# Optimization experiments

Measured on AMD Instinct MI355X. Metric: run time of the kernel, lower is better.

## Reference

```python
import jax, jax.numpy as jnp
import numpy as np

IN_DIM = 128
OUT_DIM = 128
DEGREE = 3
BATCH = 8192


def setup_inputs() -> dict:
    key = jax.random.key(0)
    k1, k2 = jax.random.split(key)
    x = jax.random.normal(k1, (BATCH, IN_DIM), dtype=jnp.float32)
    # coeff ~ 0.1*randn, shape [out_dim*in_dim, degree+1]
    coeff = 0.1 * jax.random.normal(k2, (OUT_DIM * IN_DIM, DEGREE + 1), dtype=jnp.float32)
    return {"x": x, "coeff": coeff}


def reference(x, coeff):
    # x: [B, in_dim], coeff: [out_dim*in_dim, D+1]
    # Original tiles x to [out_dim*in_dim, B]; edge i = (o*in_dim + j) uses x[:, j].
    # out[i,b] = sum_d coeff[i,d] * x[b, i % in_dim]**d, then sum over in_dim.
    B, in_dim = x.shape
    D1 = coeff.shape[-1]
    out_dim = coeff.shape[0] // in_dim
    exps = jnp.arange(D1, dtype=x.dtype)
    powed = x[:, :, None] ** exps            # [B, in_dim, D+1]
    c = coeff.reshape(out_dim, in_dim, D1)    # [out_dim, in_dim, D+1]
    # per-edge polynomial eval fused with sum over in_dim
    y = jnp.einsum('bid,oid->bo', powed, c)   # [B, out_dim]
    return y
```

## Files before the change

kernel.cpp:

```cpp
#include <hip/hip_runtime.h>


#define BATCH   8192
#define IN_DIM  128
#define OUT_DIM 128
#define KDIM    512

typedef __attribute__((ext_vector_type(8))) short bf16x8;
typedef __attribute__((ext_vector_type(4))) float f32x4;

__device__ inline unsigned short f2bf(float f) {
    union { float f; unsigned int u; } v; v.f = f;
    unsigned int u = v.u;
    u += 0x7FFFu + ((u >> 16) & 1u);
    return (unsigned short)(u >> 16);
}

#if defined(__has_builtin)
#if __has_builtin(__builtin_amdgcn_cvt_pk_bf16_f32)
#define HAVE_HW_PKBF16 1
#endif
#endif

#ifdef HAVE_HW_PKBF16
typedef __attribute__((ext_vector_type(2))) __bf16 bf16x2_t;
__device__ inline unsigned int pk2(float a, float b) {
    bf16x2_t r = __builtin_amdgcn_cvt_pk_bf16_f32(a, b);
    union { bf16x2_t v; unsigned int u; } c; c.v = r; return c.u;
}
#else
__device__ inline unsigned int pk2(float a, float b) {
    return (unsigned int)f2bf(a) | ((unsigned int)f2bf(b) << 16);
}
#endif

__global__ __launch_bounds__(256) void kan_prep(const float* __restrict__ coeff,
                                                unsigned int* __restrict__ wbf) {
    const int i = (blockIdx.x * 256 + threadIdx.x) * 4;
    const float4 c = *(const float4*)(coeff + i);
    uint2 o;
    o.x = pk2(c.x, c.y);
    o.y = pk2(c.z, c.w);
    *(uint2*)(wbf + i / 2) = o;
}

__global__ __launch_bounds__(64) void kan_mfma(const float* __restrict__ x,
                                               const unsigned short* __restrict__ wbf,
                                               float* __restrict__ out) {
    const int lane = threadIdx.x;
    const int q    = lane >> 4;
    const int r    = lane & 15;
    const int m0   = blockIdx.x * 16;
    const int n0   = blockIdx.y * 16;

    const float*          xrow = x   + (size_t)(m0 + r) * IN_DIM;
    const unsigned short* wrow = wbf + (size_t)(n0 + r) * KDIM;

    f32x4 acc = {0.f, 0.f, 0.f, 0.f};

    #pragma unroll
    for (int s = 0; s < KDIM / 32; ++s) {
        const bf16x8 bw = *(const bf16x8*)(wrow + s * 32 + q * 8);

        const float2 xv = *(const float2*)(xrow + s * 8 + q * 2);
        const float x0 = xv.x, x1 = xv.y;
        union { unsigned int u[4]; bf16x8 v; } af;
        af.u[0] = pk2(1.0f, x0);
        af.u[1] = pk2(x0 * x0, x0 * x0 * x0);
        af.u[2] = pk2(1.0f, x1);
        af.u[3] = pk2(x1 * x1, x1 * x1 * x1);

        acc = __builtin_amdgcn_mfma_f32_16x16x32_bf16(af.v, bw, acc, 0, 0, 0);
    }

    float* orow = out + (size_t)(m0 + q * 4) * OUT_DIM + n0 + r;
    #pragma unroll
    for (int rr = 0; rr < 4; ++rr) {
        orow[rr * OUT_DIM] = acc[rr];
    }
}

extern "C" void kernel_launch(void* const* d_in, const int* in_sizes, int n_in,
                              void* d_out, int out_size, void* d_ws, size_t ws_size,
                              hipStream_t stream) {
    const float* x     = (const float*)d_in[0];
    const float* coeff = (const float*)d_in[1];
    float* out = (float*)d_out;

    unsigned int* wbf = (unsigned int*)d_ws;

    kan_prep<<<OUT_DIM * KDIM / (256 * 4), 256, 0, stream>>>(coeff, wbf);

    dim3 grid(BATCH / 16, OUT_DIM / 16);
    kan_mfma<<<grid, 64, 0, stream>>>(x, (const unsigned short*)wbf, out);
}
```

Before: 72.21 us.

## Fuse coefficient bf16 conversion into MFMA kernel and tile two N blocks

Drops the separate prep kernel that converted coeff to bf16 in workspace. The main kernel now loads fp32 coefficients directly and converts them in registers. Each wave also computes two 16-wide output tiles, so the x-power fragment is reused across two MFMAs and the grid is halved in N. This removes a kernel launch and a workspace round trip, but doubles coefficient bytes read per block and repeats the conversion in every block.

```diff
diff --git a/kernel.cpp b/kernel.cpp
--- a/kernel.cpp
+++ b/kernel.cpp
@@ -34,49 +34,61 @@
 }
 #endif
 
-__global__ __launch_bounds__(256) void kan_prep(const float* __restrict__ coeff,
-                                                unsigned int* __restrict__ wbf) {
-    const int i = (blockIdx.x * 256 + threadIdx.x) * 4;
-    const float4 c = *(const float4*)(coeff + i);
-    uint2 o;
-    o.x = pk2(c.x, c.y);
-    o.y = pk2(c.z, c.w);
-    *(uint2*)(wbf + i / 2) = o;
+union frag_u { unsigned int u[4]; bf16x8 v; };
+
+__device__ inline bf16x8 cvt_frag(const float4 a, const float4 b) {
+    frag_u f;
+    f.u[0] = pk2(a.x, a.y);
+    f.u[1] = pk2(a.z, a.w);
+    f.u[2] = pk2(b.x, b.y);
+    f.u[3] = pk2(b.z, b.w);
+    return f.v;
 }
 
 __global__ __launch_bounds__(64) void kan_mfma(const float* __restrict__ x,
-                                               const unsigned short* __restrict__ wbf,
+                                               const float* __restrict__ coeff,
                                                float* __restrict__ out) {
     const int lane = threadIdx.x;
     const int q    = lane >> 4;
     const int r    = lane & 15;
     const int m0   = blockIdx.x * 16;
-    const int n0   = blockIdx.y * 16;
+    const int n0   = blockIdx.y * 32;
 
-    const float*          xrow = x   + (size_t)(m0 + r) * IN_DIM;
-    const unsigned short* wrow = wbf + (size_t)(n0 + r) * KDIM;
+    const float* xrow  = x     + (size_t)(m0 + r) * IN_DIM;
+    const float* w0row = coeff + (size_t)(n0 + r) * KDIM;
+    const float* w1row = coeff + (size_t)(n0 + 16 + r) * KDIM;
 
-    f32x4 acc = {0.f, 0.f, 0.f, 0.f};
+    f32x4 acc0 = {0.f, 0.f, 0.f, 0.f};
+    f32x4 acc1 = {0.f, 0.f, 0.f, 0.f};
 
     #pragma unroll
     for (int s = 0; s < KDIM / 32; ++s) {
-        const bf16x8 bw = *(const bf16x8*)(wrow + s * 32 + q * 8);
+        const int ko = s * 32 + q * 8;
+        const float4 b0a = *(const float4*)(w0row + ko);
+        const float4 b0b = *(const float4*)(w0row + ko + 4);
+        const float4 b1a = *(const float4*)(w1row + ko);
+        const float4 b1b = *(const float4*)(w1row + ko + 4);
 
         const float2 xv = *(const float2*)(xrow + s * 8 + q * 2);
         const float x0 = xv.x, x1 = xv.y;
-        union { unsigned int u[4]; bf16x8 v; } af;
+        frag_u af;
         af.u[0] = pk2(1.0f, x0);
         af.u[1] = pk2(x0 * x0, x0 * x0 * x0);
         af.u[2] = pk2(1.0f, x1);
         af.u[3] = pk2(x1 * x1, x1 * x1 * x1);
 
-        acc = __builtin_amdgcn_mfma_f32_16x16x32_bf16(af.v, bw, acc, 0, 0, 0);
+        const bf16x8 bf0 = cvt_frag(b0a, b0b);
+        const bf16x8 bf1 = cvt_frag(b1a, b1b);
+
+        acc0 = __builtin_amdgcn_mfma_f32_16x16x32_bf16(af.v, bf0, acc0, 0, 0, 0);
+        acc1 = __builtin_amdgcn_mfma_f32_16x16x32_bf16(af.v, bf1, acc1, 0, 0, 0);
     }
 
     float* orow = out + (size_t)(m0 + q * 4) * OUT_DIM + n0 + r;
     #pragma unroll
     for (int rr = 0; rr < 4; ++rr) {
-        orow[rr * OUT_DIM] = acc[rr];
+        orow[rr * OUT_DIM]      = acc0[rr];
+        orow[rr * OUT_DIM + 16] = acc1[rr];
     }
 }
 
@@ -87,10 +99,6 @@
     const float* coeff = (const float*)d_in[1];
     float* out = (float*)d_out;
 
-    unsigned int* wbf = (unsigned int*)d_ws;
-
-    kan_prep<<<OUT_DIM * KDIM / (256 * 4), 256, 0, stream>>>(coeff, wbf);
-
-    dim3 grid(BATCH / 16, OUT_DIM / 16);
-    kan_mfma<<<grid, 64, 0, stream>>>(x, (const unsigned short*)wbf, out);
+    dim3 grid(BATCH / 16, OUT_DIM / 32);
+    kan_mfma<<<grid, 64, 0, stream>>>(x, coeff, out);
 }
```

Measured after the change: 74.11 us. 1.03x slower.

## Fuse coeff conversion into LDS-tiled MFMA kernel with double-buffered power tiles

Applied to the files above, without the earlier changes.

Removes the separate coeff-to-bf16 prep kernel and instead has each block convert its 32-row coeff slice into LDS. Blocks now cover 64x32 outputs with 4 waves, computing x powers once per tile into double-buffered LDS and reusing them across two MFMA accumulators. The intent is to cut launch overhead and redundant global loads and power computation. The cost is redundant coeff conversion in every block, more LDS use and block-level syncs.

```diff
diff --git a/kernel.cpp b/kernel.cpp
--- a/kernel.cpp
+++ b/kernel.cpp
@@ -5,6 +5,12 @@
 #define IN_DIM  128
 #define OUT_DIM 128
 #define KDIM    512
+#define M_BLK   64
+#define N_BLK   32
+#define BK      128
+#define NSTAGE  (KDIM / BK)
+#define WPAD    520
+#define APAD    136
 
 typedef __attribute__((ext_vector_type(8))) short bf16x8;
 typedef __attribute__((ext_vector_type(4))) float f32x4;
@@ -34,49 +40,86 @@
 }
 #endif
 
-__global__ __launch_bounds__(256) void kan_prep(const float* __restrict__ coeff,
-                                                unsigned int* __restrict__ wbf) {
-    const int i = (blockIdx.x * 256 + threadIdx.x) * 4;
-    const float4 c = *(const float4*)(coeff + i);
-    uint2 o;
-    o.x = pk2(c.x, c.y);
-    o.y = pk2(c.z, c.w);
-    *(uint2*)(wbf + i / 2) = o;
+__device__ inline void write_pow4(unsigned short* dst, const float4 v) {
+    unsigned int o[8];
+    o[0] = pk2(1.0f, v.x); o[1] = pk2(v.x * v.x, v.x * v.x * v.x);
+    o[2] = pk2(1.0f, v.y); o[3] = pk2(v.y * v.y, v.y * v.y * v.y);
+    o[4] = pk2(1.0f, v.z); o[5] = pk2(v.z * v.z, v.z * v.z * v.z);
+    o[6] = pk2(1.0f, v.w); o[7] = pk2(v.w * v.w, v.w * v.w * v.w);
+    *(uint4*)(dst)     = *(uint4*)&o[0];
+    *(uint4*)(dst + 8) = *(uint4*)&o[4];
 }
 
-__global__ __launch_bounds__(64) void kan_mfma(const float* __restrict__ x,
-                                               const unsigned short* __restrict__ wbf,
-                                               float* __restrict__ out) {
-    const int lane = threadIdx.x;
+__global__ __launch_bounds__(256) void kan_mfma(const float* __restrict__ x,
+                                                const float* __restrict__ coeff,
+                                                float* __restrict__ out) {
+    __shared__ __align__(16) unsigned short W_lds[N_BLK * WPAD];
+    __shared__ __align__(16) unsigned short A_lds[2][M_BLK * APAD];
+
+    const int t    = threadIdx.x;
+    const int w    = t >> 6;
+    const int lane = t & 63;
     const int q    = lane >> 4;
     const int r    = lane & 15;
-    const int m0   = blockIdx.x * 16;
-    const int n0   = blockIdx.y * 16;
-
-    const float*          xrow = x   + (size_t)(m0 + r) * IN_DIM;
-    const unsigned short* wrow = wbf + (size_t)(n0 + r) * KDIM;
-
-    f32x4 acc = {0.f, 0.f, 0.f, 0.f};
+    const int m0   = blockIdx.x * M_BLK;
+    const int n0   = blockIdx.y * N_BLK;
 
     #pragma unroll
-    for (int s = 0; s < KDIM / 32; ++s) {
-        const bf16x8 bw = *(const bf16x8*)(wrow + s * 32 + q * 8);
-
-        const float2 xv = *(const float2*)(xrow + s * 8 + q * 2);
-        const float x0 = xv.x, x1 = xv.y;
-        union { unsigned int u[4]; bf16x8 v; } af;
-        af.u[0] = pk2(1.0f, x0);
-        af.u[1] = pk2(x0 * x0, x0 * x0 * x0);
-        af.u[2] = pk2(1.0f, x1);
-        af.u[3] = pk2(x1 * x1, x1 * x1 * x1);
-
-        acc = __builtin_amdgcn_mfma_f32_16x16x32_bf16(af.v, bw, acc, 0, 0, 0);
+    for (int i = 0; i < 16; ++i) {
+        const int f    = i * 256 + t;
+        const int row  = f >> 7;
+        const int col4 = f & 127;
+        const float4 c = *(const float4*)&coeff[(size_t)(n0 + row) * KDIM + col4 * 4];
+        uint2 o;
+        o.x = pk2(c.x, c.y);
+        o.y = pk2(c.z, c.w);
+        *(uint2*)&W_lds[row * WPAD + col4 * 4] = o;
     }
 
-    float* orow = out + (size_t)(m0 + q * 4) * OUT_DIM + n0 + r;
+    const int xr0 = t >> 3;
+    const int xr1 = (t + 256) >> 3;
+    const int xc4 = t & 7;
+
+    float4 p0 = *(const float4*)&x[(size_t)(m0 + xr0) * IN_DIM + xc4 * 4];
+    float4 p1 = *(const float4*)&x[(size_t)(m0 + xr1) * IN_DIM + xc4 * 4];
+    write_pow4(&A_lds[0][xr0 * APAD + xc4 * 16], p0);
+    write_pow4(&A_lds[0][xr1 * APAD + xc4 * 16], p1);
+    __syncthreads();
+
+    f32x4 acc0 = {0.f, 0.f, 0.f, 0.f};
+    f32x4 acc1 = {0.f, 0.f, 0.f, 0.f};
+
+    for (int s = 0; s < NSTAGE; ++s) {
+        if (s + 1 < NSTAGE) {
+            const int jc = (s + 1) * 32;
+            p0 = *(const float4*)&x[(size_t)(m0 + xr0) * IN_DIM + jc + xc4 * 4];
+            p1 = *(const float4*)&x[(size_t)(m0 + xr1) * IN_DIM + jc + xc4 * 4];
+        }
+
+        const unsigned short* Ab = A_lds[s & 1];
+        #pragma unroll
+        for (int u = 0; u < BK / 32; ++u) {
+            const int ko = u * 32 + q * 8;
+            const bf16x8 av = *(const bf16x8*)&Ab[(w * 16 + r) * APAD + ko];
+            const bf16x8 b0 = *(const bf16x8*)&W_lds[r        * WPAD + s * BK + ko];
+            const bf16x8 b1 = *(const bf16x8*)&W_lds[(16 + r) * WPAD + s * BK + ko];
+            acc0 = __builtin_amdgcn_mfma_f32_16x16x32_bf16(av, b0, acc0, 0, 0, 0);
+            acc1 = __builtin_amdgcn_mfma_f32_16x16x32_bf16(av, b1, acc1, 0, 0, 0);
+        }
+
+        if (s + 1 < NSTAGE) {
+            unsigned short* An = A_lds[(s + 1) & 1];
+            write_pow4(&An[xr0 * APAD + xc4 * 16], p0);
+            write_pow4(&An[xr1 * APAD + xc4 * 16], p1);
+            __syncthreads();
+        }
+    }
+
+    float* obase = out + (size_t)(m0 + w * 16 + q * 4) * OUT_DIM + n0 + r;
     #pragma unroll
     for (int rr = 0; rr < 4; ++rr) {
-        orow[rr * OUT_DIM] = acc[rr];
+        obase[rr * OUT_DIM]      = acc0[rr];
+        obase[rr * OUT_DIM + 16] = acc1[rr];
     }
 }
 
@@ -87,10 +130,6 @@
     const float* coeff = (const float*)d_in[1];
     float* out = (float*)d_out;
 
-    unsigned int* wbf = (unsigned int*)d_ws;
-
-    kan_prep<<<OUT_DIM * KDIM / (256 * 4), 256, 0, stream>>>(coeff, wbf);
-
-    dim3 grid(BATCH / 16, OUT_DIM / 16);
-    kan_mfma<<<grid, 64, 0, stream>>>(x, (const unsigned short*)wbf, out);
+    dim3 grid(BATCH / M_BLK, OUT_DIM / N_BLK);
+    kan_mfma<<<grid, 256, 0, stream>>>(x, coeff, out);
 }
```

After: 61.55 us. 1.17x faster.
